# Kernel tuning notes

Measured on AMD Instinct MI355X. Metric: run time of the kernel, lower is better.

Reference implementation:

```python
import jax, jax.numpy as jnp
import numpy as np

N_NODES = 100000
N_GRAPHS = 512
IN_CH, HID, OUT_CH = 128, 32, 10
N_EDGES = 3200000


def gcn_conv(x, src, dst, norm, W, b, n_nodes):
    # h = X W  (transform first: PyG GCNConv does lin() before propagate)
    h = x @ W                                   # [N, F_out]
    # gather source features, scale by symmetric norm, scatter-add to targets
    msgs = h[src] * norm[:, None]               # [E+N, F_out]
    out = jax.ops.segment_sum(msgs, dst, num_segments=n_nodes)
    return out + b


def _sym_norm(edge_index, n_nodes):
    # add self-loops, compute D^{-1/2} (A+I) D^{-1/2} edge weights
    loops = jnp.arange(n_nodes, dtype=edge_index.dtype)
    src = jnp.concatenate([edge_index[0], loops])
    dst = jnp.concatenate([edge_index[1], loops])
    deg = jax.ops.segment_sum(jnp.ones_like(dst, dtype=jnp.float32), dst,
                              num_segments=n_nodes)
    dinv = jnp.where(deg > 0, jax.lax.rsqrt(jnp.maximum(deg, 1.0)), 0.0)
    norm = dinv[src] * dinv[dst]
    return src, dst, norm


def setup_inputs() -> dict:
    key = jax.random.key(0)
    ks = jax.random.split(key, 12)
    x = jax.random.normal(ks[0], (N_NODES, IN_CH), dtype=jnp.float32)
    edge_index = jax.random.randint(ks[1], (2, N_EDGES), 0, N_NODES, dtype=jnp.int64)
    batch = jnp.sort(jax.random.randint(ks[2], (N_NODES,), 0, N_GRAPHS, dtype=jnp.int64))
    def glorot(k, fi, fo):
        lim = np.sqrt(6.0 / (fi + fo)).astype(np.float32)
        return jax.random.uniform(k, (fi, fo), jnp.float32, -lim, lim)
    return {
        "x": x, "edge_index": edge_index, "batch": batch,
        "W1": glorot(ks[3], IN_CH, HID), "b1": jnp.zeros((HID,), jnp.float32),
        "W2": glorot(ks[4], HID, HID),   "b2": jnp.zeros((HID,), jnp.float32),
        "W3": glorot(ks[5], HID, HID),   "b3": jnp.zeros((HID,), jnp.float32),
        "Wl": glorot(ks[6], HID, OUT_CH), "bl": jnp.zeros((OUT_CH,), jnp.float32),
    }


def reference(x, edge_index, batch, W1, b1, W2, b2, W3, b3, Wl, bl):
    n_nodes = x.shape[0]
    src, dst, norm = _sym_norm(edge_index, n_nodes)
    h = gcn_conv(x, src, dst, norm, W1, b1, n_nodes)
    h = jax.nn.relu(h)
    h = gcn_conv(h, src, dst, norm, W2, b2, n_nodes)
    h = jax.nn.relu(h)
    h = gcn_conv(h, src, dst, norm, W3, b3, n_nodes)  # no relu on last layer
    # global mean pool over graphs in the batch
    sums = jax.ops.segment_sum(h, batch, num_segments=N_GRAPHS)   # [G, HID]
    cnts = jax.ops.segment_sum(jnp.ones((n_nodes,), jnp.float32), batch,
                               num_segments=N_GRAPHS)
    emb = sums / jnp.maximum(cnts, 1.0)[:, None]
    # dropout(p=0.5) is identity in eval mode
    return emb @ Wl + bl
```

## Files before the change

### kernel.cpp

```cpp
#include <hip/hip_runtime.h>
#include <hip/hip_bf16.h>
#include <hip/hip_fp16.h>

#define N_NODES  100000
#define N_GRAPHS 512
#define IN_CH    128
#define HID      32
#define OUT_CH   10
#define N_EDGES  3200000

#define SZC   256
#define NBC   ((N_NODES + SZC - 1) / SZC)
#define CAPC  9216
#define SLAB  10240
#define RND   8192
#define BKT   1024
#define EPT   8
#define NRND  ((N_EDGES + RND - 1) / RND)

typedef _Float16 half8 __attribute__((ext_vector_type(8)));
typedef float    f32x4 __attribute__((ext_vector_type(4)));

__device__ __forceinline__ int load_idx(const int* __restrict__ p, long long pos, int is64) {
  return is64 ? p[2 * pos] : p[(int)pos];
}

__device__ __forceinline__ void h8_acc(float4 raw, float* a) {
  const __half2* ph = (const __half2*)&raw;
#pragma unroll
  for (int q = 0; q < 4; q++) {
    float2 f = __half22float2(ph[q]);
    a[2 * q]     += f.x;
    a[2 * q + 1] += f.y;
  }
}

__global__ void setup_k(const int* __restrict__ ei, const int* __restrict__ batch,
                        const float* __restrict__ W1, const float* __restrict__ W2,
                        const float* __restrict__ W3, __half* __restrict__ P1,
                        __half* __restrict__ P2, __half* __restrict__ P3,
                        int* __restrict__ flag, int* __restrict__ gcur) {
  __shared__ int any_nz;
  int b = blockIdx.x, t = threadIdx.x;
  if (b < 2) {
    const int* buf = (b == 0) ? ei : batch;
    if (t == 0) any_nz = 0;
    __syncthreads();
    for (int i = t; i < 4096; i += 256) {
      if (buf[2 * i + 1] != 0) any_nz = 1;
    }
    __syncthreads();
    if (t == 0) flag[b] = any_nz ? 0 : 1;
  } else {
    for (int i = t; i < NBC; i += 256) gcur[i] = 0;
    for (int idx = t; idx < 4 * 2 * 64 * 8; idx += 256) {
      int j = idx & 7, l = (idx >> 3) & 63, ct = (idx >> 9) & 1, s = idx >> 10;
      int k = s * 32 + (l >> 4) * 8 + j, c = ct * 16 + (l & 15);
      P1[idx] = __float2half(W1[k * 32 + c]);
    }
    for (int idx = t; idx < 2 * 64 * 8; idx += 256) {
      int j = idx & 7, l = (idx >> 3) & 63, ct = (idx >> 9) & 1;
      int k = (l >> 4) * 8 + j, c = ct * 16 + (l & 15);
      P2[idx] = __float2half(W2[k * 32 + c]);
      P3[idx] = __float2half(W3[k * 32 + c]);
    }
  }
}

__global__ void bucket_k(const int* __restrict__ ei, const int* __restrict__ flag,
                         int* __restrict__ gcur, int* __restrict__ bstore) {
  __shared__ int hist[NBC];
  __shared__ int base[NBC];
  int is64 = flag[0];
  int t = threadIdx.x;
  int rd = blockIdx.x;
  for (int i = t; i < NBC; i += BKT) hist[i] = 0;
  __syncthreads();
  long long e0 = (long long)rd * RND;
  int   pk[EPT];
  short cb[EPT];
#pragma unroll
  for (int k = 0; k < EPT / 2; k++) {
    long long e = e0 + (long long)(k * BKT + t) * 2;
    if (e < N_EDGES) {
      int s0, s1, d0, d1;
      if (is64) {
        int4 sv = *(const int4*)(ei + 2 * e);
        int4 dv = *(const int4*)(ei + 2 * (N_EDGES + e));
        s0 = sv.x; s1 = sv.z; d0 = dv.x; d1 = dv.z;
      } else {
        int2 sv = *(const int2*)(ei + e);
        int2 dv = *(const int2*)(ei + N_EDGES + e);
        s0 = sv.x; s1 = sv.y; d0 = dv.x; d1 = dv.y;
      }
      pk[2 * k]     = (s0 << 8) | (d0 & 255);
      cb[2 * k]     = (short)(d0 >> 8);
      pk[2 * k + 1] = (s1 << 8) | (d1 & 255);
      cb[2 * k + 1] = (short)(d1 >> 8);
      atomicAdd(&hist[d0 >> 8], 1);
      atomicAdd(&hist[d1 >> 8], 1);
    } else {
      cb[2 * k]     = -1;
      cb[2 * k + 1] = -1;
    }
  }
  __syncthreads();
  for (int c = t; c < NBC; c += BKT) {
    int h = hist[c];
    if (h > 0) base[c] = atomicAdd(&gcur[c], h);
  }
  __syncthreads();
#pragma unroll
  for (int k = 0; k < EPT; k++) {
    if (cb[k] >= 0) {
      int c = cb[k];
      int pos = atomicAdd(&base[c], 1);
      if (pos < CAPC) bstore[(size_t)c * CAPC + pos] = pk[k];
    }
  }
}

__global__ void build_csr(const int* __restrict__ bstore, const int* __restrict__ gcur,
                          int* __restrict__ csr, int* __restrict__ row_ptr,
                          int* __restrict__ deg, float* __restrict__ dinv) {
  __shared__ int hist[SZC];
  __shared__ int sc[SZC];
  __shared__ int cur[SZC];
  int b = blockIdx.x, t = threadIdx.x;
  hist[t] = 0;
  __syncthreads();
  int cnt = min(gcur[b], CAPC);
  const int* eb = bstore + (size_t)b * CAPC;
  for (int i = t; i < cnt; i += 256) atomicAdd(&hist[eb[i] & 255], 1);
  __syncthreads();
  int own = hist[t];
  int pd  = (own + 3) & ~3;
  sc[t] = pd;
  __syncthreads();
  for (int off = 1; off < SZC; off <<= 1) {
    int u = (t >= off) ? sc[t - off] : 0;
    __syncthreads();
    sc[t] += u;
    __syncthreads();
  }
  int excl = sc[t] - pd;
  int gbase = b * SLAB;
  int node = b * SZC + t;
  if (node < N_NODES) {
    row_ptr[node] = gbase + excl;
    deg[node]     = own;
    dinv[node]    = rsqrtf((float)(own + 1));
  }
  cur[t] = excl;
  __syncthreads();
  for (int i = t; i < cnt; i += 256) {
    int pk = eb[i];
    int pos = atomicAdd(&cur[pk & 255], 1);
    csr[gbase + pos] = pk >> 8;
  }
}

template <int K>
__global__ void gemm_mfma(const float* __restrict__ X, const __half* __restrict__ P,
                          const float* __restrict__ dinv, __half* __restrict__ G) {
  int wid  = threadIdx.x >> 6;
  int lane = threadIdx.x & 63;
  int row0 = (blockIdx.x * 4 + wid) * 16;
  if (row0 >= N_NODES) return;
  int r  = lane & 15;
  int ko = lane >> 4;
  f32x4 acc0 = {0.f, 0.f, 0.f, 0.f};
  f32x4 acc1 = {0.f, 0.f, 0.f, 0.f};
  const float* xrow = X + (size_t)(row0 + r) * K + ko * 8;
#pragma unroll
  for (int s = 0; s < K / 32; s++) {
    float4 xa = *(const float4*)(xrow + s * 32);
    float4 xb = *(const float4*)(xrow + s * 32 + 4);
    half8 a;
    a[0] = (_Float16)xa.x; a[1] = (_Float16)xa.y;
    a[2] = (_Float16)xa.z; a[3] = (_Float16)xa.w;
    a[4] = (_Float16)xb.x; a[5] = (_Float16)xb.y;
    a[6] = (_Float16)xb.z; a[7] = (_Float16)xb.w;
    half8 b0 = *(const half8*)(P + ((size_t)(s * 2 + 0) * 64 + lane) * 8);
    half8 b1 = *(const half8*)(P + ((size_t)(s * 2 + 1) * 64 + lane) * 8);
    acc0 = __builtin_amdgcn_mfma_f32_16x16x32_f16(a, b0, acc0, 0, 0, 0);
    acc1 = __builtin_amdgcn_mfma_f32_16x16x32_f16(a, b1, acc1, 0, 0, 0);
  }
  int col   = lane & 15;
  int rbase = row0 + (lane >> 4) * 4;
#pragma unroll
  for (int i = 0; i < 4; i++) {
    float dn = dinv[rbase + i];
    G[(size_t)(rbase + i) * 32 + col]      = __float2half(acc0[i] * dn);
    G[(size_t)(rbase + i) * 32 + 16 + col] = __float2half(acc1[i] * dn);
  }
}

__global__ void agg_pull(const __half* __restrict__ g, const int* __restrict__ csr,
                         const int* __restrict__ row_ptr, const int* __restrict__ deg,
                         const float* __restrict__ dinv, const float* __restrict__ bias,
                         float* __restrict__ out, int do_relu) {
  int node = blockIdx.x * 32 + (threadIdx.x >> 3);
  if (node >= N_NODES) return;
  int half = (threadIdx.x >> 2) & 1;
  int j    = threadIdx.x & 3;
  const __half* gj = g + j * 8;
  int base = row_ptr[node];
  int n    = deg[node];
  int nh   = ((n >> 1) + 3) & ~3;
  if (nh > n) nh = n;
  int lo = half ? nh : 0;
  int hi = half ? n : nh;
  float a0[8] = {0.f, 0.f, 0.f, 0.f, 0.f, 0.f, 0.f, 0.f};
  float a1[8] = {0.f, 0.f, 0.f, 0.f, 0.f, 0.f, 0.f, 0.f};
  int i = lo;
  for (; i + 3 < hi; i += 4) {
    int4 s4 = *(const int4*)(csr + base + i);
    float4 r0 = *(const float4*)(gj + (size_t)s4.x * HID);
    float4 r1 = *(const float4*)(gj + (size_t)s4.y * HID);
    float4 r2 = *(const float4*)(gj + (size_t)s4.z * HID);
    float4 r3 = *(const float4*)(gj + (size_t)s4.w * HID);
    h8_acc(r0, a0);
    h8_acc(r1, a1);
    h8_acc(r2, a0);
    h8_acc(r3, a1);
  }
  for (; i < hi; i++) {
    int s0 = csr[base + i];
    h8_acc(*(const float4*)(gj + (size_t)s0 * HID), a0);
  }
#pragma unroll
  for (int k = 0; k < 8; k++) a0[k] += a1[k];
#pragma unroll
  for (int k = 0; k < 8; k++) a0[k] += __shfl_xor(a0[k], 4, 64);
  if (half == 0) {
    float self[8] = {0.f, 0.f, 0.f, 0.f, 0.f, 0.f, 0.f, 0.f};
    h8_acc(*(const float4*)(gj + (size_t)node * HID), self);
    float dnv = dinv[node];
    float4 bb0 = *(const float4*)(bias + j * 8);
    float4 bb1 = *(const float4*)(bias + j * 8 + 4);
    float bbv[8] = {bb0.x, bb0.y, bb0.z, bb0.w, bb1.x, bb1.y, bb1.z, bb1.w};
    float r[8];
#pragma unroll
    for (int k = 0; k < 8; k++) {
      r[k] = dnv * (a0[k] + self[k]) + bbv[k];
      if (do_relu) r[k] = fmaxf(r[k], 0.f);
    }
    *(float4*)(out + (size_t)node * HID + j * 8)     = make_float4(r[0], r[1], r[2], r[3]);
    *(float4*)(out + (size_t)node * HID + j * 8 + 4) = make_float4(r[4], r[5], r[6], r[7]);
  }
}

__global__ void pool_head(const float* __restrict__ h, const int* __restrict__ batch,
                          const int* __restrict__ flag, const float* __restrict__ Wl,
                          const float* __restrict__ bl, float* __restrict__ out) {
  __shared__ float acc[8][HID];
  int g = blockIdx.x, t = threadIdx.x;
  int is64 = flag[1];
  int start, end;
  {
    int lo = 0, hi = N_NODES;
    while (lo < hi) { int m = (lo + hi) >> 1; if (load_idx(batch, m, is64) < g) lo = m + 1; else hi = m; }
    start = lo;
    lo = start; hi = N_NODES;
    while (lo < hi) { int m = (lo + hi) >> 1; if (load_idx(batch, m, is64) < g + 1) lo = m + 1; else hi = m; }
    end = lo;
  }
  int c = t & 31, r = t >> 5;
  float s = 0.f;
  for (int i = start + r; i < end; i += 8) s += h[(size_t)i * HID + c];
  acc[r][c] = s;
  __syncthreads();
  if (t < HID) {
    float v = 0.f;
#pragma unroll
    for (int q = 0; q < 8; q++) v += acc[q][t];
    acc[0][t] = v / fmaxf((float)(end - start), 1.0f);
  }
  __syncthreads();
  if (t < OUT_CH) {
    float o = bl[t];
#pragma unroll
    for (int k = 0; k < HID; k++) o += acc[0][k] * Wl[k * OUT_CH + t];
    out[g * OUT_CH + t] = o;
  }
}

extern "C" void kernel_launch(void* const* d_in, const int* in_sizes, int n_in,
                              void* d_out, int out_size, void* d_ws, size_t ws_size,
                              hipStream_t stream) {
  const float* x   = (const float*)d_in[0];
  const int* ei    = (const int*)d_in[1];
  const int* batch = (const int*)d_in[2];
  const float* W1  = (const float*)d_in[3];
  const float* b1  = (const float*)d_in[4];
  const float* W2  = (const float*)d_in[5];
  const float* b2  = (const float*)d_in[6];
  const float* W3  = (const float*)d_in[7];
  const float* b3  = (const float*)d_in[8];
  const float* Wl  = (const float*)d_in[9];
  const float* bl  = (const float*)d_in[10];
  float* out = (float*)d_out;

  char* p = (char*)d_ws;
  auto alloc = [&](size_t bytes) {
    void* r = (void*)p;
    p += (bytes + 255) & ~(size_t)255;
    return r;
  };
  int*    gcur    = (int*)alloc((size_t)NBC * 4);
  int*    bstore  = (int*)alloc((size_t)NBC * CAPC * 4);
  int*    csr     = (int*)alloc((size_t)NBC * SLAB * 4);
  int*    row_ptr = (int*)alloc((size_t)N_NODES * 4);
  int*    deg     = (int*)alloc((size_t)N_NODES * 4);
  float*  dinv    = (float*)alloc((size_t)N_NODES * 4);
  int*    flag    = (int*)alloc(8);
  __half* g       = (__half*)alloc((size_t)N_NODES * HID * 2);
  float*  h       = (float*)alloc((size_t)N_NODES * HID * 4);
  __half* P1      = (__half*)alloc((size_t)4 * 2 * 64 * 8 * 2);
  __half* P2      = (__half*)alloc((size_t)2 * 64 * 8 * 2);
  __half* P3      = (__half*)alloc((size_t)2 * 64 * 8 * 2);

  setup_k<<<3, 256, 0, stream>>>(ei, batch, W1, W2, W3, P1, P2, P3, flag, gcur);
  bucket_k<<<NRND, BKT, 0, stream>>>(ei, flag, gcur, bstore);
  build_csr<<<NBC, 256, 0, stream>>>(bstore, gcur, csr, row_ptr, deg, dinv);

  const int GB = (N_NODES / 16 + 3) / 4;
  const int AB = (N_NODES + 31) / 32;
  gemm_mfma<IN_CH><<<GB, 256, 0, stream>>>(x, P1, dinv, g);
  agg_pull<<<AB, 256, 0, stream>>>(g, csr, row_ptr, deg, dinv, b1, h, 1);
  gemm_mfma<HID><<<GB, 256, 0, stream>>>(h, P2, dinv, g);
  agg_pull<<<AB, 256, 0, stream>>>(g, csr, row_ptr, deg, dinv, b2, h, 1);
  gemm_mfma<HID><<<GB, 256, 0, stream>>>(h, P3, dinv, g);
  agg_pull<<<AB, 256, 0, stream>>>(g, csr, row_ptr, deg, dinv, b3, h, 0);

  pool_head<<<N_GRAPHS, 256, 0, stream>>>(h, batch, flag, Wl, bl, out);
}
```

Baseline: 225.8 us.

## Fuse next-layer 32x32 transform into aggregation kernel epilogue

The layer-2 and layer-3 GEMMs are folded into the epilogue of the preceding aggregation kernel. Each block stages its 32 aggregated rows and W in shared memory, does a small FP32 matmul, scales by dinv and writes fp16 features for the next layer. This drops two kernel launches and the fp32 h write and re-read between layers, at the cost of a syncthreads, extra shared memory and ping-pong feature buffers. The node bounds check is removed, which relies on N_NODES being divisible by 32.

```diff
diff --git a/kernel.cpp b/kernel.cpp
--- a/kernel.cpp
+++ b/kernel.cpp
@@ -36,9 +36,7 @@
 }
 
 __global__ void setup_k(const int* __restrict__ ei, const int* __restrict__ batch,
-                        const float* __restrict__ W1, const float* __restrict__ W2,
-                        const float* __restrict__ W3, __half* __restrict__ P1,
-                        __half* __restrict__ P2, __half* __restrict__ P3,
+                        const float* __restrict__ W1, __half* __restrict__ P1,
                         int* __restrict__ flag, int* __restrict__ gcur) {
   __shared__ int any_nz;
   int b = blockIdx.x, t = threadIdx.x;
@@ -57,12 +55,6 @@
       int j = idx & 7, l = (idx >> 3) & 63, ct = (idx >> 9) & 1, s = idx >> 10;
       int k = s * 32 + (l >> 4) * 8 + j, c = ct * 16 + (l & 15);
       P1[idx] = __float2half(W1[k * 32 + c]);
-    }
-    for (int idx = t; idx < 2 * 64 * 8; idx += 256) {
-      int j = idx & 7, l = (idx >> 3) & 63, ct = (idx >> 9) & 1;
-      int k = (l >> 4) * 8 + j, c = ct * 16 + (l & 15);
-      P2[idx] = __float2half(W2[k * 32 + c]);
-      P3[idx] = __float2half(W3[k * 32 + c]);
     }
   }
 }
@@ -196,14 +188,21 @@
   }
 }
 
+template <int FUSE>
 __global__ void agg_pull(const __half* __restrict__ g, const int* __restrict__ csr,
                          const int* __restrict__ row_ptr, const int* __restrict__ deg,
                          const float* __restrict__ dinv, const float* __restrict__ bias,
-                         float* __restrict__ out, int do_relu) {
-  int node = blockIdx.x * 32 + (threadIdx.x >> 3);
-  if (node >= N_NODES) return;
-  int half = (threadIdx.x >> 2) & 1;
-  int j    = threadIdx.x & 3;
+                         const float* __restrict__ Wn, __half* __restrict__ gout,
+                         float* __restrict__ hout, int do_relu) {
+  __shared__ float hh[32][33];
+  __shared__ float Ws[32 * 32];
+  int t = threadIdx.x;
+  if (FUSE) {
+    for (int i = t; i < 1024; i += 256) Ws[i] = Wn[i];
+  }
+  int node = blockIdx.x * 32 + (t >> 3);
+  int half = (t >> 2) & 1;
+  int j    = t & 3;
   const __half* gj = g + j * 8;
   int base = row_ptr[node];
   int n    = deg[node];
@@ -246,8 +245,29 @@
       r[k] = dnv * (a0[k] + self[k]) + bbv[k];
       if (do_relu) r[k] = fmaxf(r[k], 0.f);
     }
-    *(float4*)(out + (size_t)node * HID + j * 8)     = make_float4(r[0], r[1], r[2], r[3]);
-    *(float4*)(out + (size_t)node * HID + j * 8 + 4) = make_float4(r[4], r[5], r[6], r[7]);
+    if (FUSE) {
+      int nl = t >> 3;
+#pragma unroll
+      for (int k = 0; k < 8; k++) hh[nl][j * 8 + k] = r[k];
+    } else {
+      *(float4*)(hout + (size_t)node * HID + j * 8)     = make_float4(r[0], r[1], r[2], r[3]);
+      *(float4*)(hout + (size_t)node * HID + j * 8 + 4) = make_float4(r[4], r[5], r[6], r[7]);
+    }
+  }
+  if (FUSE) {
+    __syncthreads();
+    int nl = t >> 3, cg = t & 7;
+    float acc0 = 0.f, acc1 = 0.f, acc2 = 0.f, acc3 = 0.f;
+#pragma unroll
+    for (int k = 0; k < 32; k++) {
+      float hv = hh[nl][k];
+      float4 w = *(const float4*)(Ws + k * 32 + cg * 4);
+      acc0 += hv * w.x; acc1 += hv * w.y; acc2 += hv * w.z; acc3 += hv * w.w;
+    }
+    float dn = dinv[node];
+    __half2* go = (__half2*)(gout + (size_t)node * 32 + cg * 4);
+    go[0] = __halves2half2(__float2half(acc0 * dn), __float2half(acc1 * dn));
+    go[1] = __halves2half2(__float2half(acc2 * dn), __float2half(acc3 * dn));
   }
 }
 
@@ -315,24 +335,21 @@
   int*    deg     = (int*)alloc((size_t)N_NODES * 4);
   float*  dinv    = (float*)alloc((size_t)N_NODES * 4);
   int*    flag    = (int*)alloc(8);
-  __half* g       = (__half*)alloc((size_t)N_NODES * HID * 2);
+  __half* gA      = (__half*)alloc((size_t)N_NODES * HID * 2);
+  __half* gB      = (__half*)alloc((size_t)N_NODES * HID * 2);
   float*  h       = (float*)alloc((size_t)N_NODES * HID * 4);
   __half* P1      = (__half*)alloc((size_t)4 * 2 * 64 * 8 * 2);
-  __half* P2      = (__half*)alloc((size_t)2 * 64 * 8 * 2);
-  __half* P3      = (__half*)alloc((size_t)2 * 64 * 8 * 2);
-
-  setup_k<<<3, 256, 0, stream>>>(ei, batch, W1, W2, W3, P1, P2, P3, flag, gcur);
+
+  setup_k<<<3, 256, 0, stream>>>(ei, batch, W1, P1, flag, gcur);
   bucket_k<<<NRND, BKT, 0, stream>>>(ei, flag, gcur, bstore);
   build_csr<<<NBC, 256, 0, stream>>>(bstore, gcur, csr, row_ptr, deg, dinv);
 
   const int GB = (N_NODES / 16 + 3) / 4;
-  const int AB = (N_NODES + 31) / 32;
-  gemm_mfma<IN_CH><<<GB, 256, 0, stream>>>(x, P1, dinv, g);
-  agg_pull<<<AB, 256, 0, stream>>>(g, csr, row_ptr, deg, dinv, b1, h, 1);
-  gemm_mfma<HID><<<GB, 256, 0, stream>>>(h, P2, dinv, g);
-  agg_pull<<<AB, 256, 0, stream>>>(g, csr, row_ptr, deg, dinv, b2, h, 1);
-  gemm_mfma<HID><<<GB, 256, 0, stream>>>(h, P3, dinv, g);
-  agg_pull<<<AB, 256, 0, stream>>>(g, csr, row_ptr, deg, dinv, b3, h, 0);
+  const int AB = N_NODES / 32;
+  gemm_mfma<IN_CH><<<GB, 256, 0, stream>>>(x, P1, dinv, gA);
+  agg_pull<1><<<AB, 256, 0, stream>>>(gA, csr, row_ptr, deg, dinv, b1, W2, gB, nullptr, 1);
+  agg_pull<1><<<AB, 256, 0, stream>>>(gB, csr, row_ptr, deg, dinv, b2, W3, gA, nullptr, 1);
+  agg_pull<0><<<AB, 256, 0, stream>>>(gA, csr, row_ptr, deg, dinv, b3, nullptr, nullptr, h, 0);
 
   pool_head<<<N_GRAPHS, 256, 0, stream>>>(h, batch, flag, Wl, bl, out);
 }
```

Measured after the change: 211.5 us. -6.3%, faster.
